# Performance work log

Hardware: AMD Instinct MI355X
Metric: run time of the kernel (lower is better)

Reference implementation:

```python
import jax, jax.numpy as jnp
import numpy as np

# --- static config matching init_kwargs ---
PATTERN_SPECS = {4: 25, 5: 25, 6: 25, 7: 25}
P = sum(PATTERN_SPECS.values())          # total_num_patterns = 100
MAXL = max(PATTERN_SPECS.keys())          # max_pattern_length = 7
D = 300                                   # embedding_dim
V = 10000                                 # local vocab size
B = 32                                    # batch size
T = 2048                                  # max_doc_len
NC = 2                                    # num_classes
BIAS_SCALE = 1.0
EPS = 1e-5
TAU = 0.0
# end state per pattern (pattern_len - 1), ordered by pattern_specs
END_IDX = np.array([l - 1 for l, n in PATTERN_SPECS.items() for _ in range(n)], dtype=np.int32)


def setup_inputs() -> dict:
    key = jax.random.key(0)
    ks = jax.random.split(key, 8)
    local_embeddings = jax.random.normal(ks[0], (D, V), jnp.float32)
    diags = jax.random.normal(ks[1], (P * (MAXL - 1), D), jnp.float32) * (2.0 / (P * (MAXL - 1) + D)) ** 0.5
    bias = jax.random.normal(ks[2], (P * (MAXL - 1), 1), jnp.float32) * 0.05
    wildcards = jax.random.normal(ks[3], (P, MAXL - 1), jnp.float32) * 0.1
    linear_w = jax.random.normal(ks[4], (NC, P), jnp.float32) * 0.1
    linear_b = jnp.zeros((NC,), jnp.float32)
    docs = jax.random.randint(ks[5], (B, T), 0, V)
    doc_lens = jax.random.randint(ks[6], (B,), T // 2, T + 1)
    return dict(local_embeddings=local_embeddings, diags=diags, bias=bias,
                wildcards=wildcards, linear_w=linear_w, linear_b=linear_b,
                docs=docs, doc_lens=doc_lens)


def masked_layer_norm(x, eps=EPS):
    # MaskedLayerNorm with mask = ~isinf(x); equals plain layer_norm when no infs.
    mask = ~jnp.isinf(x)
    masked = jnp.where(mask, x, 0.0)
    divisor = jnp.sum(mask, axis=1, keepdims=True).astype(x.dtype)
    mean = jnp.sum(masked, axis=1, keepdims=True) / divisor
    var = jnp.sum(jnp.where(mask, (masked - mean) ** 2, 0.0), axis=1, keepdims=True) / divisor
    normalized = (masked - mean) / jnp.sqrt(var + eps)
    return jnp.where(mask, normalized, x)


def reference(local_embeddings, diags, bias, wildcards, linear_w, linear_b, docs, doc_lens):
    # MaxSum semiring: zero=-inf, one=0, plus=max, times=+, identity outer maps.
    # transition scores per local token: [V, P*(MAXL-1)] -> gather per doc token
    trans = (diags @ local_embeddings + BIAS_SCALE * bias).T          # [V, P*(L-1)]
    tm = trans[docs].reshape(B, T, P, MAXL - 1)                        # [B,T,P,L-1]
    wc = wildcards[None]                                               # wildcard_scale = semiring.one = 0
    end_idx = jnp.asarray(END_IDX)
    pidx = jnp.arange(P)

    restart = jnp.zeros((B, P, 1), tm.dtype)                           # semiring.one
    h0 = jnp.concatenate([restart, jnp.full((B, P, MAXL - 1), -jnp.inf, tm.dtype)], axis=2)
    s0 = jnp.full((B, P), -jnp.inf, tm.dtype)                          # semiring.zero
    tm_seq = jnp.moveaxis(tm, 1, 0)                                    # [T,B,P,L-1]

    def step(carry, inp):
        scores, hiddens = carry
        tmt, t = inp
        prev = hiddens[:, :, :-1]                                      # [B,P,L-1]
        main = jnp.concatenate([restart, prev + tmt], axis=2)          # semiring.times
        wild = jnp.concatenate([restart, prev + wc], axis=2)
        hiddens = jnp.maximum(main, wild)                              # semiring.plus
        end_vals = hiddens[:, pidx, end_idx]                           # gather end states [B,P]
        active = (doc_lens > t)[:, None]
        scores = jnp.where(active, jnp.maximum(scores, end_vals), scores)
        return (scores, hiddens), None

    (scores, _), _ = jax.lax.scan(step, (s0, h0), (tm_seq, jnp.arange(T)))

    scores = masked_layer_norm(scores)
    scores = (scores > TAU).astype(scores.dtype)                       # STE binarizer (forward)
    return scores @ linear_w.T + linear_b
```

## Files before the change

### kernel.cpp

```cpp
#include <hip/hip_runtime.h>
#include <hip/hip_bf16.h>
#include <cmath>
#include <cstdint>

#define V_   10000
#define D_   300
#define P_   100
#define B_   32
#define T_   2048
#define NC_  2
#define CP_  450
#define CPAD 464

__device__ __constant__ int GC0c[9] = {0, 57, 107, 159, 215, 270, 330, 390, 450};
__device__ __constant__ int GP0c[9] = {0, 19, 33, 46, 58, 69, 80, 90, 100};

__device__ __forceinline__ int maprow(int c) {
    if (c < 75)  return (c / 3) * 6 + c % 3;
    if (c < 175) { int q = c - 75;  return (25 + q / 4) * 6 + q % 4; }
    if (c < 300) { int q = c - 175; return (50 + q / 5) * 6 + q % 5; }
    int q = c - 300; return (75 + q / 6) * 6 + q % 6;
}
__device__ __forceinline__ int cstart(int p) {
    if (p < 25) return 3 * p;
    if (p < 50) return 75 + 4 * (p - 25);
    if (p < 75) return 175 + 5 * (p - 50);
    return 300 + 6 * (p - 75);
}

__global__ __launch_bounds__(256) void k_tr(const float* __restrict__ diags,
                                            const float* __restrict__ bias,
                                            const float* __restrict__ wc,
                                            float* __restrict__ dT,
                                            float* __restrict__ bp,
                                            float* __restrict__ wp) {
    const int idx = blockIdx.x * 256 + threadIdx.x;
    if (idx < CPAD) {
        float b = 0.f, w = 0.f;
        if (idx < CP_) { int r = maprow(idx); b = bias[r]; w = wc[r]; }
        bp[idx] = b; wp[idx] = w;
    }
    if (idx < D_ * CPAD) {
        const int d = idx / CPAD, cp = idx - d * CPAD;
        dT[idx] = (cp < CP_) ? diags[maprow(cp) * D_ + d] : 0.f;
    }
}

__global__ __launch_bounds__(256) void k_gemm(const float* __restrict__ emb,
                                              const float* __restrict__ dT,
                                              const float* __restrict__ bp,
                                              const float* __restrict__ wp,
                                              float* __restrict__ mt) {
    const int bid = blockIdx.x;
    const int xcd = bid & 7, ii = bid >> 3;
    const int ord = xcd * 145 + ii;
    const int vt = ord / 29, ct = ord - vt * 29;
    const int cb = ct * 16;
    const int tid = threadIdx.x;
    const int v = vt * 256 + tid;
    const int vc = min(v, V_ - 1);

    const float* ep = emb + vc;
    const float* dr = dT + cb;

    float acc[16] = {};
    float evA[6], evB[6];
    #pragma unroll
    for (int u = 0; u < 6; ++u) evA[u] = ep[(size_t)u * V_];

    #pragma unroll 2
    for (int g = 0; g < 50; ++g) {
        const int d0 = g * 6;
        if (g < 49) {
            #pragma unroll
            for (int u = 0; u < 6; ++u) evB[u] = ep[(size_t)(d0 + 6 + u) * V_];
        }
        #pragma unroll
        for (int u = 0; u < 6; ++u) {
            const float* dg = dr + (size_t)(d0 + u) * CPAD;
            #pragma unroll
            for (int j = 0; j < 16; ++j)
                acc[j] = fmaf(evA[u], dg[j], acc[j]);
        }
        #pragma unroll
        for (int u = 0; u < 6; ++u) evA[u] = evB[u];
    }

    if (v < V_) {
        #pragma unroll
        for (int j = 0; j < 16; ++j)
            acc[j] = fmaxf(acc[j] + bp[cb + j], wp[cb + j]);
        float* op = mt + (size_t)v * CPAD + cb;
        #pragma unroll
        for (int q = 0; q < 4; ++q)
            *(float4*)(op + q * 4) = make_float4(acc[q*4], acc[q*4+1],
                                                 acc[q*4+2], acc[q*4+3]);
    }
}

#define SROW 69
#define SST  65

__global__ __launch_bounds__(256) void k_scan(const float* __restrict__ mt,
                                              const int* __restrict__ docs,
                                              const int* __restrict__ doc_lens,
                                              float* __restrict__ part) {
    __shared__ float sm[SROW * SST];
    __shared__ int rowbuf[SROW];
    const int bid = blockIdx.x;
    const int pg = bid & 7;
    const int ts = (bid >> 3) & 31;
    const int b  = bid >> 8;
    const int ts0 = ts * 64;
    const int len = doc_lens[b];
    if (ts0 + 3 > len) return;
    const int tid = threadIdx.x;
    const int lane = tid & 63, wid = tid >> 6;
    const int nst = min(SROW, min(T_ - ts0, len - ts0));
    const int c0 = GC0c[pg];
    const int c0a = c0 & ~3;
    const int cg = GC0c[pg + 1] - c0;
    const int nf4 = (c0 - c0a + cg + 3) >> 2;

    for (int q = tid; q < nst; q += 256) rowbuf[q] = docs[b * T_ + ts0 + q];
    __syncthreads();
    for (int q = tid; q < (nst << 4); q += 256) {
        const int r = q >> 4, c4 = q & 15;
        if (c4 < nf4) {
            const float4 vv = *(const float4*)(mt + (size_t)rowbuf[r] * CPAD
                                               + c0a + (c4 << 2));
            const int base = r * SST + (c4 << 2);
            sm[base]     = vv.x;
            sm[base + 1] = vv.y;
            sm[base + 2] = vv.z;
            sm[base + 3] = vv.w;
        }
    }
    __syncthreads();

    const int t = lane;
    for (int p = GP0c[pg] + wid; p < GP0c[pg + 1]; p += 4) {
        const int e = 3 + p / 25;
        const int cbs = cstart(p) - c0a;
        float s = sm[t * SST + cbs];
        for (int i = 1; i < e; ++i) s += sm[(t + i) * SST + cbs + i];
        float val = (ts0 + t + e <= len) ? s : -INFINITY;
        #pragma unroll
        for (int off = 32; off > 0; off >>= 1)
            val = fmaxf(val, __shfl_xor(val, off, 64));
        if (lane == 0) part[((size_t)b * 32 + ts) * P_ + p] = val;
    }
}

__global__ __launch_bounds__(128) void k_final(const float* __restrict__ part,
                                               const int* __restrict__ doc_lens,
                                               const float* __restrict__ lw,
                                               const float* __restrict__ lb,
                                               float* __restrict__ out) {
    const int b = blockIdx.x;
    const int tid = threadIdx.x;
    __shared__ float sh[P_];
    __shared__ float stats[2];

    const int len = doc_lens[b];
    const int nseg = min(32, (len - 3) / 64 + 1);

    float s = -INFINITY;
    bool fin = false;
    if (tid < P_) {
        for (int sg = 0; sg < nseg; ++sg)
            s = fmaxf(s, part[((size_t)b * 32 + sg) * P_ + tid]);
        fin = !isinf(s);
        sh[tid] = s;
    }
    __syncthreads();
    if (tid == 0) {
        int n = 0; float sum = 0.f;
        for (int p = 0; p < P_; p++) {
            float x = sh[p];
            if (!isinf(x)) { n++; sum += x; }
        }
        float mean = sum / (float)n;
        float var = 0.f;
        for (int p = 0; p < P_; p++) {
            float x = sh[p];
            if (!isinf(x)) { float d = x - mean; var += d * d; }
        }
        var /= (float)n;
        stats[0] = mean;
        stats[1] = 1.f / sqrtf(var + 1e-5f);
    }
    __syncthreads();
    if (tid < P_) {
        float norm = fin ? (s - stats[0]) * stats[1] : s;
        sh[tid] = (norm > 0.f) ? 1.f : 0.f;
    }
    __syncthreads();
    if (tid < NC_) {
        float accv = lb[tid];
        for (int p = 0; p < P_; p++) accv += sh[p] * lw[tid * P_ + p];
        out[b * NC_ + tid] = accv;
    }
}

extern "C" void kernel_launch(void* const* d_in, const int* in_sizes, int n_in,
                              void* d_out, int out_size, void* d_ws, size_t ws_size,
                              hipStream_t stream) {
    const float* emb   = (const float*)d_in[0];
    const float* diags = (const float*)d_in[1];
    const float* bias  = (const float*)d_in[2];
    const float* wc    = (const float*)d_in[3];
    const float* lw    = (const float*)d_in[4];
    const float* lb    = (const float*)d_in[5];
    const int*   docs  = (const int*)d_in[6];
    const int*   dlens = (const int*)d_in[7];
    float* out = (float*)d_out;

    float* mt   = (float*)d_ws;
    float* dT   = mt + (size_t)V_ * CPAD;
    float* bp   = dT + (size_t)D_ * CPAD;
    float* wp   = bp + CPAD;
    float* part = wp + CPAD;

    k_tr   <<<dim3(544),  256, 0, stream>>>(diags, bias, wc, dT, bp, wp);
    k_gemm <<<dim3(1160), 256, 0, stream>>>(emb, dT, bp, wp, mt);
    k_scan <<<dim3(8192), 256, 0, stream>>>(mt, docs, dlens, part);
    k_final<<<dim3(B_),   128, 0, stream>>>(part, dlens, lw, lb, out);
}
```

Baseline: 154.8 us.

## Make scan blocks persistent over 16 segments with register-staged double buffering

The scan kernel now launches 512 blocks, each covering 16 consecutive 64-token segments, instead of one block per segment. While one segment is computed from shared memory, the gathered rows for the next segment are prefetched into registers and then written into an alternate shared buffer. This amortizes block launch and setup and overlaps gather latency with compute. The trade-offs are less parallelism (512 blocks of 256 threads on a 256-CU part), higher register and shared-memory use, and serialized segments inside each block.

Result: slower. 229.3 us (+48.1%).

```diff
diff --git a/kernel.cpp b/kernel.cpp
--- a/kernel.cpp
+++ b/kernel.cpp
@@ -100,55 +100,84 @@
 
 #define SROW 69
 #define SST  65
+#define UPT  5
 
 __global__ __launch_bounds__(256) void k_scan(const float* __restrict__ mt,
                                               const int* __restrict__ docs,
                                               const int* __restrict__ doc_lens,
                                               float* __restrict__ part) {
-    __shared__ float sm[SROW * SST];
-    __shared__ int rowbuf[SROW];
+    __shared__ float sm[2][SROW * SST];
     const int bid = blockIdx.x;
     const int pg = bid & 7;
-    const int ts = (bid >> 3) & 31;
-    const int b  = bid >> 8;
-    const int ts0 = ts * 64;
+    const int half = (bid >> 3) & 1;
+    const int b = bid >> 4;
     const int len = doc_lens[b];
-    if (ts0 + 3 > len) return;
+    const int ts_beg = half * 16, ts_end = ts_beg + 16;
+    if (ts_beg * 64 + 3 > len) return;
     const int tid = threadIdx.x;
     const int lane = tid & 63, wid = tid >> 6;
-    const int nst = min(SROW, min(T_ - ts0, len - ts0));
     const int c0 = GC0c[pg];
     const int c0a = c0 & ~3;
     const int cg = GC0c[pg + 1] - c0;
     const int nf4 = (c0 - c0a + cg + 3) >> 2;
 
-    for (int q = tid; q < nst; q += 256) rowbuf[q] = docs[b * T_ + ts0 + q];
-    __syncthreads();
-    for (int q = tid; q < (nst << 4); q += 256) {
-        const int r = q >> 4, c4 = q & 15;
-        if (c4 < nf4) {
-            const float4 vv = *(const float4*)(mt + (size_t)rowbuf[r] * CPAD
-                                               + c0a + (c4 << 2));
-            const int base = r * SST + (c4 << 2);
-            sm[base]     = vv.x;
-            sm[base + 1] = vv.y;
-            sm[base + 2] = vv.z;
-            sm[base + 3] = vv.w;
-        }
-    }
-    __syncthreads();
-
-    const int t = lane;
-    for (int p = GP0c[pg] + wid; p < GP0c[pg + 1]; p += 4) {
-        const int e = 3 + p / 25;
-        const int cbs = cstart(p) - c0a;
-        float s = sm[t * SST + cbs];
-        for (int i = 1; i < e; ++i) s += sm[(t + i) * SST + cbs + i];
-        float val = (ts0 + t + e <= len) ? s : -INFINITY;
-        #pragma unroll
-        for (int off = 32; off > 0; off >>= 1)
-            val = fmaxf(val, __shfl_xor(val, off, 64));
-        if (lane == 0) part[((size_t)b * 32 + ts) * P_ + p] = val;
+    int ur[UPT], uc4[UPT];
+    bool uv[UPT];
+    #pragma unroll
+    for (int k = 0; k < UPT; ++k) {
+        const int u = tid + (k << 8);
+        ur[k] = u >> 4; uc4[k] = u & 15;
+        uv[k] = (u < SROW * 16) && (uc4[k] < nf4);
+    }
+
+    float4 stg[UPT];
+    {
+        const int ts0 = ts_beg * 64;
+        const int nst = min(SROW, min(T_ - ts0, len - ts0));
+        #pragma unroll
+        for (int k = 0; k < UPT; ++k)
+            if (uv[k] && ur[k] < nst) {
+                const int row = docs[b * T_ + ts0 + ur[k]];
+                stg[k] = *(const float4*)(mt + (size_t)row * CPAD + c0a + (uc4[k] << 2));
+            }
+    }
+
+    for (int ts = ts_beg; ts < ts_end; ++ts) {
+        const int ts0 = ts * 64;
+        if (ts0 + 3 > len) break;
+        const int nst = min(SROW, min(T_ - ts0, len - ts0));
+        const int cur = ts & 1;
+
+        #pragma unroll
+        for (int k = 0; k < UPT; ++k)
+            if (uv[k] && ur[k] < nst)
+                *(float4*)&sm[cur][ur[k] * SST + (uc4[k] << 2)] = stg[k];
+        __syncthreads();
+
+        const int nts0 = ts0 + 64;
+        if (ts + 1 < ts_end && nts0 + 3 <= len) {
+            const int nnst = min(SROW, min(T_ - nts0, len - nts0));
+            #pragma unroll
+            for (int k = 0; k < UPT; ++k)
+                if (uv[k] && ur[k] < nnst) {
+                    const int row = docs[b * T_ + nts0 + ur[k]];
+                    stg[k] = *(const float4*)(mt + (size_t)row * CPAD + c0a + (uc4[k] << 2));
+                }
+        }
+
+        const int t = lane;
+        for (int p = GP0c[pg] + wid; p < GP0c[pg + 1]; p += 4) {
+            const int e = 3 + p / 25;
+            const int cbs = cstart(p) - c0a;
+            float s = sm[cur][t * SST + cbs];
+            for (int i = 1; i < e; ++i) s += sm[cur][(t + i) * SST + cbs + i];
+            float val = (ts0 + t + e <= len) ? s : -INFINITY;
+            #pragma unroll
+            for (int off = 32; off > 0; off >>= 1)
+                val = fmaxf(val, __shfl_xor(val, off, 64));
+            if (lane == 0) part[((size_t)b * 32 + ts) * P_ + p] = val;
+        }
+        __syncthreads();
     }
 }
 
@@ -224,6 +253,6 @@
 
     k_tr   <<<dim3(544),  256, 0, stream>>>(diags, bias, wc, dT, bp, wp);
     k_gemm <<<dim3(1160), 256, 0, stream>>>(emb, dT, bp, wp, mt);
-    k_scan <<<dim3(8192), 256, 0, stream>>>(mt, docs, dlens, part);
+    k_scan <<<dim3(512),  256, 0, stream>>>(mt, docs, dlens, part);
     k_final<<<dim3(B_),   128, 0, stream>>>(part, dlens, lw, lb, out);
 }
```
